# Kernel tuning notes

Measured on AMD Instinct MI355X. Metric: run time of the kernel, lower is better.

## Reference

```python
import jax, jax.numpy as jnp
import numpy as np

VOLRADIUS = 256.0
DT = 1.0 / VOLRADIUS  # self.dt = dt / volradius with dt=1.0
N_STEPS = 64
B, H, W, K, M = 1, 256, 256, 64, 16


def setup_inputs() -> dict:
    rng = np.random.default_rng(0)
    # orthographic-ish ray bundle looking down +z through the primitive cloud
    ys, xs = np.meshgrid(np.linspace(-1., 1., H, dtype=np.float32),
                         np.linspace(-1., 1., W, dtype=np.float32), indexing='ij')
    raypos = np.broadcast_to(np.stack([xs, ys, np.full_like(xs, -0.125)], -1)[None],
                             (B, H, W, 3)).astype(np.float32).copy()
    raydir = np.zeros((B, H, W, 3), np.float32); raydir[..., 2] = 1.0
    tmin = np.zeros((B, H, W), np.float32)
    tminmax = np.stack([tmin, tmin + N_STEPS * DT], -1).astype(np.float32)
    # primpos is in WORLD units (module divides by volradius)
    primpos = rng.uniform(-0.1 * VOLRADIUS, 0.1 * VOLRADIUS, (B, K, 3)).astype(np.float32)
    q, _ = np.linalg.qr(rng.normal(size=(B, K, 3, 3)))
    primrot = q.astype(np.float32)
    primscale = rng.uniform(8., 16., (B, K, 3)).astype(np.float32)  # inverse half-extent
    primrgba = rng.uniform(0., 1., (B, K, 4, M, M, M)).astype(np.float32)
    return {
        'raypos': jnp.asarray(raypos), 'raydir': jnp.asarray(raydir),
        'tminmax': jnp.asarray(tminmax), 'primpos': jnp.asarray(primpos),
        'primrot': jnp.asarray(primrot), 'primscale': jnproundtrip(primscale) if False else jnp.asarray(primscale),
        'primrgba': jnp.asarray(primrgba),
    }


def _trilinear_sum(template, pos, primpos, primrot, primscale):
    # template [K,4,M,M,M]; pos [R,3]; returns summed rgba over primitives [R,4]
    Mv = template.shape[-1]
    kidx = jnp.arange(template.shape[0])[None, :]                      # [1,K]
    rel = pos[:, None, :] - primpos[None, :, :]                        # [R,K,3]
    # local = primscale * (primrot^T @ rel), inside prim iff |local| < 1
    local = jnp.einsum('kij,rki->rkj', primrot, rel) * primscale[None]  # [R,K,3]
    inside = jnp.all(jnp.abs(local) < 1.0, axis=-1)                    # [R,K]
    g = jnp.clip((local + 1.0) * 0.5 * (Mv - 1), 0.0, Mv - 1 - 1e-5)    # voxel coords (x,y,z)
    i0 = jnp.clip(jnp.floor(g).astype(jnp.int32), 0, Mv - 2)
    f = g - i0.astype(g.dtype)
    x0, y0, z0 = i0[..., 0], i0[..., 1], i0[..., 2]
    fx, fy, fz = f[..., 0], f[..., 1], f[..., 2]
    c = jnp.zeros(local.shape[:2] + (4,), template.dtype)
    for dz, wz in ((0, 1 - fz), (1, fz)):
        for dy, wy in ((0, 1 - fy), (1, fy)):
            for dx, wx in ((0, 1 - fx), (1, fx)):
                corner = template[kidx, :, z0 + dz, y0 + dy, x0 + dx]  # [R,K,4]
                c = c + corner * (wz * wy * wx)[..., None]
    c = c * inside[..., None]
    return c.sum(axis=1)                                               # [R,4]


def _march(raypos, raydir, tminmax, primpos, primrot, primscale, template):
    Hh, Ww, _ = raypos.shape
    R = Hh * Ww
    o = raypos.reshape(R, 3)
    d = raydir.reshape(R, 3)
    tmm = tminmax.reshape(R, 2)
    tmin, tmax = tmm[:, 0], tmm[:, 1]

    def step(carry, i):
        rgb, alpha = carry
        t = tmin + (i.astype(jnp.float32) + 0.5) * DT
        valid = t < tmax
        pos = o + t[:, None] * d
        s = _trilinear_sum(template, pos, primpos, primrot, primscale)  # [R,4]
        # MVP front-to-back saturating alpha compositing (early-term equivalent)
        contrib = jnp.minimum(1.0, alpha + s[:, 3] * DT) - alpha
        contrib = jnp.where(valid, contrib, 0.0)
        rgb = rgb + s[:, :3] * contrib[:, None]
        alpha = alpha + contrib
        return (rgb, alpha), None

    init = (jnp.zeros((R, 3), jnp.float32), jnp.zeros((R,), jnp.float32))
    (rgb, alpha), _ = jax.lax.scan(jax.checkpoint(step), init, jnp.arange(N_STEPS))
    return jnp.concatenate([rgb, alpha[:, None]], -1).reshape(Hh, Ww, 4)


def reference(raypos, raydir, tminmax, primpos, primrot, primscale, primrgba):
    primpos_n = primpos / VOLRADIUS  # module normalizes primpos by volume radius
    rayrgba = jax.vmap(_march)(raypos, raydir, tminmax, primpos_n, primrot, primscale, primrgba)
    rayrgba = jnp.transpose(rayrgba, (0, 3, 1, 2))  # [B,4,H,W]
    rayrgb = rayrgba[:, :3]
    rayalpha = rayrgba[:, 3:4]
    return rayrgb, rayalpha, rayrgba
```

## Files before the change

### kernel.cpp

```cpp
#include <hip/hip_runtime.h>
#include <hip/hip_fp16.h>

#define Rtot 65536
#define Wimg 256
#define Kp 64
#define NSTEPS 64
#define DTc (1.0f/256.0f)
#define INV_VOLR (1.0f/256.0f)
#define NITEMS 16384

#define PD_OFF    0u
#define TB_OFF    4096u
#define FLAG_OFF  20480u
#define TT_OFF    65536u
#define SBUF_OFF  8388608u
#define WS_NEED   (SBUF_OFF + (size_t)NITEMS*256*8)

typedef _Float16 half2v __attribute__((ext_vector_type(2)));

__device__ __forceinline__ half2v u2h(unsigned int u) {
  union { unsigned int u; half2v h; } x; x.u = u; return x.h;
}
__device__ __forceinline__ half2v mkh2(float a, float b) {
  half2v h; h.x = (_Float16)a; h.y = (_Float16)b; return h;
}
__device__ __forceinline__ unsigned int pack2(float a, float b) {
  __half2 h = __floats2half2_rn(a, b);
  return *(unsigned int*)&h;
}

#if __has_builtin(__builtin_amdgcn_fdot2)
#define FDOT2(a, b, c) __builtin_amdgcn_fdot2((a), (b), (c), false)
#else
#define FDOT2(a, b, c) ((float)(a).x*(float)(b).x + (float)(a).y*(float)(b).y + (c))
#endif

__global__ __launch_bounds__(256) void setup_kernel(
    const float* __restrict__ raypos, const float* __restrict__ raydir,
    const float* __restrict__ tminmax, const float* __restrict__ primpos,
    const float* __restrict__ primrot, const float* __restrict__ primscale,
    const float* __restrict__ tmpl,
    float* __restrict__ tb, uint4* __restrict__ tth, float* __restrict__ pd) {
  int bid = blockIdx.x, tid = threadIdx.x;
  if (bid < 256) {
    __shared__ float smn[4][7], smx[4][7];
    int w = (bid & 15)*16 + (tid & 15);
    int h = (bid >> 4)*16 + (tid >> 4);
    int r = h*Wimg + w;
    float v[7];
    v[0] = raypos[r*3+0]; v[1] = raypos[r*3+1]; v[2] = raypos[r*3+2];
    v[3] = raydir[r*3+0]; v[4] = raydir[r*3+1]; v[5] = raydir[r*3+2];
    v[6] = tminmax[r*2+0];
    float mn[7], mx[7];
#pragma unroll
    for (int i = 0; i < 7; ++i) { mn[i] = v[i]; mx[i] = v[i]; }
#pragma unroll
    for (int m = 1; m < 64; m <<= 1) {
#pragma unroll
      for (int i = 0; i < 7; ++i) {
        mn[i] = fminf(mn[i], __shfl_xor(mn[i], m));
        mx[i] = fmaxf(mx[i], __shfl_xor(mx[i], m));
      }
    }
    int wv = tid >> 6;
    if ((tid & 63) == 0) {
#pragma unroll
      for (int i = 0; i < 7; ++i) { smn[wv][i] = mn[i]; smx[wv][i] = mx[i]; }
    }
    __syncthreads();
    if (tid == 0) {
#pragma unroll
      for (int i = 0; i < 7; ++i) {
        tb[bid*16 + i]     = fminf(fminf(smn[0][i], smn[1][i]), fminf(smn[2][i], smn[3][i]));
        tb[bid*16 + 8 + i] = fmaxf(fmaxf(smx[0][i], smx[1][i]), fmaxf(smx[2][i], smx[3][i]));
      }
    }
  } else if (bid < 320) {
    int k = bid - 256;
    const float* b0 = tmpl + (((size_t)k) << 14);
    uint4* o = tth + (k << 12);
    for (int v = tid; v < 4096; v += 256) {
      int x = v & 15;
      int xn = (x < 15) ? v + 1 : v;
      uint4 q;
      q.x = pack2(b0[v],         b0[xn]);
      q.y = pack2(b0[4096+v],    b0[4096+xn]);
      q.z = pack2(b0[8192+v],    b0[8192+xn]);
      q.w = pack2(b0[12288+v],   b0[12288+xn]);
      o[v] = q;
    }
  } else {
    int k = tid;
    if (k < Kp) {
      float sc0 = primscale[k*3+0], sc1 = primscale[k*3+1], sc2 = primscale[k*3+2];
      float* o = pd + (k << 4);
      o[0] = primpos[k*3+0] * INV_VOLR;
      o[1] = primpos[k*3+1] * INV_VOLR;
      o[2] = primpos[k*3+2] * INV_VOLR;
      o[3] = 0.0f; o[4] = 0.0f; o[5] = 0.0f;
#pragma unroll
      for (int i = 0; i < 3; ++i) {
        o[6+i*3+0] = primrot[k*9+i*3+0]*sc0;
        o[6+i*3+1] = primrot[k*9+i*3+1]*sc1;
        o[6+i*3+2] = primrot[k*9+i*3+2]*sc2;
      }
      o[15] = 0.0f;
    }
  }
}

#define PRIM_SETUP(S, kk, vm)                                                \
  { const float* p = pd + ((kk) << 4);                                       \
    float relx = px - p[0], rely = py - p[1], relz = pz - p[2];              \
    float lx = relx*p[6] + rely*p[9]  + relz*p[12];                          \
    float ly = relx*p[7] + rely*p[10] + relz*p[13];                          \
    float lz = relx*p[8] + rely*p[11] + relz*p[14];                          \
    bool inside = fabsf(lx) < 1.0f && fabsf(ly) < 1.0f && fabsf(lz) < 1.0f;  \
    float gx = fminf(fmaxf((lx + 1.0f)*7.5f, 0.0f), 14.99999f);              \
    float gy = fminf(fmaxf((ly + 1.0f)*7.5f, 0.0f), 14.99999f);              \
    float gz = fminf(fmaxf((lz + 1.0f)*7.5f, 0.0f), 14.99999f);              \
    int ix = (int)gx, iy = (int)gy, iz = (int)gz;                            \
    float fx = gx - (float)ix, fy = gy - (float)iy, fz = gz - (float)iz;     \
    float m = inside ? (vm) : 0.0f;                                          \
    float wy0 = 1.0f - fy, wz0m = (1.0f - fz)*m, fzm = fz*m;                 \
    float wx0 = 1.0f - fx;                                                   \
    float w00 = wz0m*wy0, w01 = wz0m*fy, w10 = fzm*wy0, w11 = fzm*fy;        \
    w2_0##S = mkh2(w00*wx0, w00*fx);                                         \
    w2_1##S = mkh2(w01*wx0, w01*fx);                                         \
    w2_2##S = mkh2(w10*wx0, w10*fx);                                         \
    w2_3##S = mkh2(w11*wx0, w11*fx);                                         \
    const uint4* a = tth + ((size_t)(kk) << 12) + (iz*256 + iy*16 + ix);     \
    q0##S = a[0]; q1##S = a[16]; q2##S = a[256]; q3##S = a[272]; }

#define PRIM_ACC(S)                                                          \
  { c0 = FDOT2(u2h(q0##S.x), w2_0##S, c0);                                   \
    c1 = FDOT2(u2h(q0##S.y), w2_0##S, c1);                                   \
    c2 = FDOT2(u2h(q0##S.z), w2_0##S, c2);                                   \
    c3 = FDOT2(u2h(q0##S.w), w2_0##S, c3);                                   \
    c0 = FDOT2(u2h(q1##S.x), w2_1##S, c0);                                   \
    c1 = FDOT2(u2h(q1##S.y), w2_1##S, c1);                                   \
    c2 = FDOT2(u2h(q1##S.z), w2_1##S, c2);                                   \
    c3 = FDOT2(u2h(q1##S.w), w2_1##S, c3);                                   \
    c0 = FDOT2(u2h(q2##S.x), w2_2##S, c0);                                   \
    c1 = FDOT2(u2h(q2##S.y), w2_2##S, c1);                                   \
    c2 = FDOT2(u2h(q2##S.z), w2_2##S, c2);                                   \
    c3 = FDOT2(u2h(q2##S.w), w2_2##S, c3);                                   \
    c0 = FDOT2(u2h(q3##S.x), w2_3##S, c0);                                   \
    c1 = FDOT2(u2h(q3##S.y), w2_3##S, c1);                                   \
    c2 = FDOT2(u2h(q3##S.z), w2_3##S, c2);                                   \
    c3 = FDOT2(u2h(q3##S.w), w2_3##S, c3); }

__global__ __launch_bounds__(256) void shade_kernel(
    const float* __restrict__ raypos, const float* __restrict__ raydir,
    const float* __restrict__ tminmax, const float* __restrict__ pd,
    const float* __restrict__ tb, const uint4* __restrict__ tth,
    unsigned long long* __restrict__ sbuf, unsigned char* __restrict__ flags) {
  __shared__ int s_any;
  __shared__ int s_list[4][66];
  int item = blockIdx.x;
  int tile = item >> 6, step = item & 63;
  int tid = threadIdx.x;
  int lane = tid & 63, wv = tid >> 6;

  if (tid < 64) {
    const float* t0 = tb + tile*16;
    float cst = ((float)step + 0.5f)*DTc;
    float tl = t0[6] + cst, th = t0[14] + cst;
    const float* p = pd + (tid << 4);
    float rlo[3], rhi[3];
#pragma unroll
    for (int a = 0; a < 3; ++a) {
      float ol = t0[a], oh = t0[8+a], dl = t0[3+a], dh = t0[11+a];
      float p1 = tl*dl, p2 = tl*dh, p3 = th*dl, p4 = th*dh;
      rlo[a] = ol + fminf(fminf(p1, p2), fminf(p3, p4)) - p[a];
      rhi[a] = oh + fmaxf(fmaxf(p1, p2), fmaxf(p3, p4)) - p[a];
    }
    bool pass = true;
#pragma unroll
    for (int j = 0; j < 3; ++j) {
      float llo = 0.f, lhi = 0.f;
#pragma unroll
      for (int a = 0; a < 3; ++a) {
        float rsc = p[6+a*3+j];
        float q1 = rlo[a]*rsc, q2 = rhi[a]*rsc;
        llo += fminf(q1, q2);
        lhi += fmaxf(q1, q2);
      }
      pass = pass && (llo < 1.0f) && (lhi > -1.0f);
    }
    unsigned long long mask = __ballot(pass);
    if (tid == 0) s_any = (mask != 0ull);
  }
  __syncthreads();
  if (!s_any) {
    if (tid == 0) flags[item] = 0;
    return;
  }
  if (tid == 0) flags[item] = 1;

  int w = (tile & 15)*16 + (tid & 15);
  int h = (tile >> 4)*16 + (tid >> 4);
  int r = h*Wimg + w;
  float t = tminmax[r*2] + ((float)step + 0.5f)*DTc;
  float px = fmaf(t, raydir[r*3+0], raypos[r*3+0]);
  float py = fmaf(t, raydir[r*3+1], raypos[r*3+1]);
  float pz = fmaf(t, raydir[r*3+2], raypos[r*3+2]);

  float bmnx = px, bmny = py, bmnz = pz, bmxx = px, bmxy = py, bmxz = pz;
#pragma unroll
  for (int m = 1; m < 64; m <<= 1) {
    bmnx = fminf(bmnx, __shfl_xor(bmnx, m));
    bmny = fminf(bmny, __shfl_xor(bmny, m));
    bmnz = fminf(bmnz, __shfl_xor(bmnz, m));
    bmxx = fmaxf(bmxx, __shfl_xor(bmxx, m));
    bmxy = fmaxf(bmxy, __shfl_xor(bmxy, m));
    bmxz = fmaxf(bmxz, __shfl_xor(bmxz, m));
  }
  {
    const float* p = pd + (lane << 4);
    float rlo0 = bmnx - p[0], rhi0 = bmxx - p[0];
    float rlo1 = bmny - p[1], rhi1 = bmxy - p[1];
    float rlo2 = bmnz - p[2], rhi2 = bmxz - p[2];
    bool pass = true;
#pragma unroll
    for (int j = 0; j < 3; ++j) {
      float a0 = p[6+j], a1 = p[9+j], a2 = p[12+j];
      float q1 = rlo0*a0, q2 = rhi0*a0;
      float llo = fminf(q1, q2), lhi = fmaxf(q1, q2);
      q1 = rlo1*a1; q2 = rhi1*a1;
      llo += fminf(q1, q2); lhi += fmaxf(q1, q2);
      q1 = rlo2*a2; q2 = rhi2*a2;
      llo += fminf(q1, q2); lhi += fmaxf(q1, q2);
      pass = pass && (llo < 1.0f) && (lhi > -1.0f);
    }
    unsigned long long mask = __ballot(pass);
    int cnt = (int)__popcll(mask);
    if (pass) {
      int pos = (int)__popcll(mask & ((1ull << lane) - 1ull));
      s_list[wv][pos] = lane;
    }
    int cntp = ((cnt + 2) / 3) * 3;
    if (lane < cntp - cnt) s_list[wv][cnt + lane] = 0;

    float c0 = 0.f, c1 = 0.f, c2 = 0.f, c3 = 0.f;
    if (cnt > 0) {
      bool anyA, anyB, anyC; (void)anyA; (void)anyB; (void)anyC;
      uint4 q0A, q1A, q2A, q3A, q0B, q1B, q2B, q3B, q0C, q1C, q2C, q3C;
      half2v w2_0A, w2_1A, w2_2A, w2_3A;
      half2v w2_0B, w2_1B, w2_2B, w2_3B;
      half2v w2_0C, w2_1C, w2_2C, w2_3C;
      int kk = __builtin_amdgcn_readfirstlane(s_list[wv][0]);
      PRIM_SETUP(A, kk, 1.0f)
      kk = __builtin_amdgcn_readfirstlane(s_list[wv][1]);
      PRIM_SETUP(B, kk, (1 < cnt) ? 1.0f : 0.0f)
      kk = __builtin_amdgcn_readfirstlane(s_list[wv][2]);
      PRIM_SETUP(C, kk, (2 < cnt) ? 1.0f : 0.0f)
      for (int i = 3; i + 2 < cntp; i += 3) {
        PRIM_ACC(A)
        kk = __builtin_amdgcn_readfirstlane(s_list[wv][i]);
        PRIM_SETUP(A, kk, (i < cnt) ? 1.0f : 0.0f)
        PRIM_ACC(B)
        kk = __builtin_amdgcn_readfirstlane(s_list[wv][i+1]);
        PRIM_SETUP(B, kk, (i+1 < cnt) ? 1.0f : 0.0f)
        PRIM_ACC(C)
        kk = __builtin_amdgcn_readfirstlane(s_list[wv][i+2]);
        PRIM_SETUP(C, kk, (i+2 < cnt) ? 1.0f : 0.0f)
      }
      PRIM_ACC(A)
      PRIM_ACC(B)
      PRIM_ACC(C)
    }
    unsigned long long pk = ((unsigned long long)pack2(c2, c3) << 32)
                          | (unsigned long long)pack2(c0, c1);
    sbuf[item*256 + tid] = pk;
  }
}

__global__ __launch_bounds__(256) void composite_kernel(
    const float* __restrict__ tminmax, const unsigned long long* __restrict__ sbuf,
    const unsigned char* __restrict__ flags, float* __restrict__ out) {
  __shared__ unsigned char s_flags[NSTEPS];
  int tid = threadIdx.x;
  int b = blockIdx.x;
  if (tid < NSTEPS) s_flags[tid] = flags[b*NSTEPS + tid];
  __syncthreads();
  int w = (b & 15)*16 + (tid & 15);
  int h = (b >> 4)*16 + (tid >> 4);
  int r = h*Wimg + w;
  float tmin = tminmax[r*2+0], tmax = tminmax[r*2+1];
  float rgb0 = 0.f, rgb1 = 0.f, rgb2 = 0.f, alpha = 0.f;
  for (int i = 0; i < NSTEPS; ++i) {
    float s0 = 0.f, s1 = 0.f, s2 = 0.f, s3 = 0.f;
    if (s_flags[i]) {
      unsigned long long pk = sbuf[(b*NSTEPS + i)*256 + tid];
      unsigned int lo = (unsigned int)pk, hi = (unsigned int)(pk >> 32);
      float2 lf = __half22float2(*(__half2*)&lo);
      float2 hf = __half22float2(*(__half2*)&hi);
      s0 = lf.x; s1 = lf.y; s2 = hf.x; s3 = hf.y;
    }
    float t = tmin + ((float)i + 0.5f)*DTc;
    float contrib = fminf(1.0f, fmaf(s3, DTc, alpha)) - alpha;
    contrib = (t < tmax) ? contrib : 0.0f;
    rgb0 = fmaf(s0, contrib, rgb0);
    rgb1 = fmaf(s1, contrib, rgb1);
    rgb2 = fmaf(s2, contrib, rgb2);
    alpha += contrib;
  }
  out[0*Rtot + r] = rgb0;
  out[1*Rtot + r] = rgb1;
  out[2*Rtot + r] = rgb2;
  out[3*Rtot + r] = alpha;
  out[4*Rtot + r] = rgb0;
  out[5*Rtot + r] = rgb1;
  out[6*Rtot + r] = rgb2;
  out[7*Rtot + r] = alpha;
}

__global__ __launch_bounds__(256) void fallback_kernel(
    const float* __restrict__ raypos, const float* __restrict__ raydir,
    const float* __restrict__ tminmax,
    const float* __restrict__ primpos, const float* __restrict__ primrot,
    const float* __restrict__ primscale, const float* __restrict__ tmpl,
    float* __restrict__ out) {
  __shared__ float s_pd[Kp][16];
  int tx = threadIdx.x, ty = threadIdx.y;
  int tid = ty*16 + tx;
  if (tid < Kp) {
    int k = tid;
    float sc0 = primscale[k*3+0], sc1 = primscale[k*3+1], sc2 = primscale[k*3+2];
    s_pd[k][0] = primpos[k*3+0]*INV_VOLR;
    s_pd[k][1] = primpos[k*3+1]*INV_VOLR;
    s_pd[k][2] = primpos[k*3+2]*INV_VOLR;
#pragma unroll
    for (int i = 0; i < 3; ++i) {
      s_pd[k][6+i*3+0] = primrot[k*9+i*3+0]*sc0;
      s_pd[k][6+i*3+1] = primrot[k*9+i*3+1]*sc1;
      s_pd[k][6+i*3+2] = primrot[k*9+i*3+2]*sc2;
    }
  }
  __syncthreads();
  int w = blockIdx.x*16 + tx, h = blockIdx.y*16 + ty;
  int r = h*Wimg + w;
  float ox = raypos[r*3+0], oy = raypos[r*3+1], oz = raypos[r*3+2];
  float dx = raydir[r*3+0], dy = raydir[r*3+1], dz = raydir[r*3+2];
  float tmin = tminmax[r*2+0], tmax = tminmax[r*2+1];
  float rgb0=0.f, rgb1=0.f, rgb2=0.f, alpha=0.f;
  for (int i = 0; i < NSTEPS; ++i) {
    float t = tmin + ((float)i + 0.5f)*DTc;
    float px = fmaf(t, dx, ox), py = fmaf(t, dy, oy), pz = fmaf(t, dz, oz);
    float c[4] = {0.f, 0.f, 0.f, 0.f};
    for (int k = 0; k < Kp; ++k) {
      const float* p = &s_pd[k][0];
      float relx = px - p[0], rely = py - p[1], relz = pz - p[2];
      float lx = relx*p[6] + rely*p[9]  + relz*p[12];
      float ly = relx*p[7] + rely*p[10] + relz*p[13];
      float lz = relx*p[8] + rely*p[11] + relz*p[14];
      if (!(fabsf(lx) < 1.0f && fabsf(ly) < 1.0f && fabsf(lz) < 1.0f)) continue;
      float gx = fminf(fmaxf((lx + 1.0f)*7.5f, 0.0f), 14.99999f);
      float gy = fminf(fmaxf((ly + 1.0f)*7.5f, 0.0f), 14.99999f);
      float gz = fminf(fmaxf((lz + 1.0f)*7.5f, 0.0f), 14.99999f);
      int ix = (int)gx, iy = (int)gy, iz = (int)gz;
      ix = ix > 14 ? 14 : ix; iy = iy > 14 ? 14 : iy; iz = iz > 14 ? 14 : iz;
      float fx = gx - (float)ix, fy = gy - (float)iy, fz = gz - (float)iz;
      float wx0 = 1.0f - fx, wy0 = 1.0f - fy, wz0 = 1.0f - fz;
      float w00 = wz0*wy0, w01 = wz0*fy, w10 = fz*wy0, w11 = fz*fy;
      const float* base = tmpl + (((size_t)k) << 14) + iz*256 + iy*16 + ix;
#pragma unroll
      for (int ch = 0; ch < 4; ++ch) {
        const float* bb = base + ch*4096;
        c[ch] += (bb[0]  *wx0 + bb[1]  *fx) * w00
               + (bb[16] *wx0 + bb[17] *fx) * w01
               + (bb[256]*wx0 + bb[257]*fx) * w10
               + (bb[272]*wx0 + bb[273]*fx) * w11;
      }
    }
    float contrib = fminf(1.0f, fmaf(c[3], DTc, alpha)) - alpha;
    contrib = (t < tmax) ? contrib : 0.0f;
    rgb0 = fmaf(c[0], contrib, rgb0);
    rgb1 = fmaf(c[1], contrib, rgb1);
    rgb2 = fmaf(c[2], contrib, rgb2);
    alpha += contrib;
  }
  out[0*Rtot + r] = rgb0;
  out[1*Rtot + r] = rgb1;
  out[2*Rtot + r] = rgb2;
  out[3*Rtot + r] = alpha;
  out[4*Rtot + r] = rgb0;
  out[5*Rtot + r] = rgb1;
  out[6*Rtot + r] = rgb2;
  out[7*Rtot + r] = alpha;
}

extern "C" void kernel_launch(void* const* d_in, const int* in_sizes, int n_in,
                              void* d_out, int out_size, void* d_ws, size_t ws_size,
                              hipStream_t stream) {
  const float* raypos    = (const float*)d_in[0];
  const float* raydir    = (const float*)d_in[1];
  const float* tminmax   = (const float*)d_in[2];
  const float* primpos   = (const float*)d_in[3];
  const float* primrot   = (const float*)d_in[4];
  const float* primscale = (const float*)d_in[5];
  const float* primrgba  = (const float*)d_in[6];
  float* out = (float*)d_out;

  if (ws_size >= WS_NEED) {
    char* ws = (char*)d_ws;
    float* pd            = (float*)(ws + PD_OFF);
    float* tb            = (float*)(ws + TB_OFF);
    unsigned char* flags = (unsigned char*)(ws + FLAG_OFF);
    uint4* tth           = (uint4*)(ws + TT_OFF);
    unsigned long long* sbuf = (unsigned long long*)(ws + SBUF_OFF);

    setup_kernel<<<321, 256, 0, stream>>>(raypos, raydir, tminmax, primpos,
                                          primrot, primscale, primrgba,
                                          tb, tth, pd);
    shade_kernel<<<NITEMS, 256, 0, stream>>>(raypos, raydir, tminmax, pd, tb,
                                             tth, sbuf, flags);
    composite_kernel<<<256, 256, 0, stream>>>(tminmax, sbuf, flags, out);
  } else {
    fallback_kernel<<<dim3(16,16), dim3(16,16), 0, stream>>>(
        raypos, raydir, tminmax, primpos, primrot, primscale, primrgba, out);
  }
}
```

Before: 73.43 us.

## Split tile culling into separate kernel and shade compacted work queue persistently

```diff
diff --git a/kernel.cpp b/kernel.cpp
--- a/kernel.cpp
+++ b/kernel.cpp
@@ -8,11 +8,15 @@
 #define DTc (1.0f/256.0f)
 #define INV_VOLR (1.0f/256.0f)
 #define NITEMS 16384
+#define HOTGRID 2048
 
 #define PD_OFF    0u
 #define TB_OFF    4096u
 #define FLAG_OFF  20480u
-#define TT_OFF    65536u
+#define QC_OFF    36864u
+#define QUEUE_OFF 40960u
+#define LIST_OFF  131072u
+#define TT_OFF    2097152u
 #define SBUF_OFF  8388608u
 #define WS_NEED   (SBUF_OFF + (size_t)NITEMS*256*8)
 
@@ -40,7 +44,8 @@
     const float* __restrict__ tminmax, const float* __restrict__ primpos,
     const float* __restrict__ primrot, const float* __restrict__ primscale,
     const float* __restrict__ tmpl,
-    float* __restrict__ tb, uint4* __restrict__ tth, float* __restrict__ pd) {
+    float* __restrict__ tb, uint4* __restrict__ tth, float* __restrict__ pd,
+    int* __restrict__ qc) {
   int bid = blockIdx.x, tid = threadIdx.x;
   if (bid < 256) {
     __shared__ float smn[4][7], smx[4][7];
@@ -75,22 +80,26 @@
         tb[bid*16 + 8 + i] = fmaxf(fmaxf(smx[0][i], smx[1][i]), fmaxf(smx[2][i], smx[3][i]));
       }
     }
-  } else if (bid < 320) {
-    int k = bid - 256;
+  } else if (bid < 512) {
+    int k = (bid - 256) >> 2;
+    int q = (bid - 256) & 3;
     const float* b0 = tmpl + (((size_t)k) << 14);
     uint4* o = tth + (k << 12);
-    for (int v = tid; v < 4096; v += 256) {
+#pragma unroll
+    for (int s = 0; s < 4; ++s) {
+      int v = q*1024 + s*256 + tid;
       int x = v & 15;
       int xn = (x < 15) ? v + 1 : v;
-      uint4 q;
-      q.x = pack2(b0[v],         b0[xn]);
-      q.y = pack2(b0[4096+v],    b0[4096+xn]);
-      q.z = pack2(b0[8192+v],    b0[8192+xn]);
-      q.w = pack2(b0[12288+v],   b0[12288+xn]);
-      o[v] = q;
+      uint4 qq;
+      qq.x = pack2(b0[v],       b0[xn]);
+      qq.y = pack2(b0[4096+v],  b0[4096+xn]);
+      qq.z = pack2(b0[8192+v],  b0[8192+xn]);
+      qq.w = pack2(b0[12288+v], b0[12288+xn]);
+      o[v] = qq;
     }
   } else {
     int k = tid;
+    if (k == Kp) qc[0] = 0;
     if (k < Kp) {
       float sc0 = primscale[k*3+0], sc1 = primscale[k*3+1], sc2 = primscale[k*3+2];
       float* o = pd + (k << 4);
@@ -106,6 +115,51 @@
       }
       o[15] = 0.0f;
     }
+  }
+}
+
+__global__ __launch_bounds__(256) void cull_kernel(
+    const float* __restrict__ pd, const float* __restrict__ tb,
+    unsigned char* __restrict__ flags, unsigned char* __restrict__ lists,
+    int* __restrict__ queue, int* __restrict__ qc) {
+  int wv = threadIdx.x >> 6, lane = threadIdx.x & 63;
+  int item = blockIdx.x*4 + wv;
+  int tile = item >> 6, step = item & 63;
+  const float* t0 = tb + tile*16;
+  float cst = ((float)step + 0.5f)*DTc;
+  float tl = t0[6] + cst, th = t0[14] + cst;
+  const float* p = pd + (lane << 4);
+  float rlo[3], rhi[3];
+#pragma unroll
+  for (int a = 0; a < 3; ++a) {
+    float ol = t0[a], oh = t0[8+a], dl = t0[3+a], dh = t0[11+a];
+    float p1 = tl*dl, p2 = tl*dh, p3 = th*dl, p4 = th*dh;
+    rlo[a] = ol + fminf(fminf(p1, p2), fminf(p3, p4)) - p[a];
+    rhi[a] = oh + fmaxf(fmaxf(p1, p2), fmaxf(p3, p4)) - p[a];
+  }
+  bool pass = true;
+#pragma unroll
+  for (int j = 0; j < 3; ++j) {
+    float llo = 0.f, lhi = 0.f;
+#pragma unroll
+    for (int a = 0; a < 3; ++a) {
+      float rsc = p[6+a*3+j];
+      float q1 = rlo[a]*rsc, q2 = rhi[a]*rsc;
+      llo += fminf(q1, q2);
+      lhi += fmaxf(q1, q2);
+    }
+    pass = pass && (llo < 1.0f) && (lhi > -1.0f);
+  }
+  unsigned long long mask = __ballot(pass);
+  int cnt = (int)__popcll(mask);
+  if (lane == 0) flags[item] = (unsigned char)(cnt > 0 ? 1 : 0);
+  if (pass) {
+    int pos = (int)__popcll(mask & ((1ull << lane) - 1ull));
+    lists[item*64 + pos] = (unsigned char)lane;
+  }
+  if (cnt > 0 && lane == 0) {
+    int qpos = atomicAdd(qc, 1);
+    queue[qpos] = item | (cnt << 16);
   }
 }
 
@@ -153,98 +207,67 @@
 __global__ __launch_bounds__(256) void shade_kernel(
     const float* __restrict__ raypos, const float* __restrict__ raydir,
     const float* __restrict__ tminmax, const float* __restrict__ pd,
-    const float* __restrict__ tb, const uint4* __restrict__ tth,
-    unsigned long long* __restrict__ sbuf, unsigned char* __restrict__ flags) {
-  __shared__ int s_any;
+    const uint4* __restrict__ tth, const unsigned char* __restrict__ lists,
+    const int* __restrict__ queue, const int* __restrict__ qc,
+    unsigned long long* __restrict__ sbuf) {
   __shared__ int s_list[4][66];
-  int item = blockIdx.x;
-  int tile = item >> 6, step = item & 63;
+  int qn = qc[0];
   int tid = threadIdx.x;
   int lane = tid & 63, wv = tid >> 6;
-
-  if (tid < 64) {
-    const float* t0 = tb + tile*16;
-    float cst = ((float)step + 0.5f)*DTc;
-    float tl = t0[6] + cst, th = t0[14] + cst;
-    const float* p = pd + (tid << 4);
-    float rlo[3], rhi[3];
-#pragma unroll
-    for (int a = 0; a < 3; ++a) {
-      float ol = t0[a], oh = t0[8+a], dl = t0[3+a], dh = t0[11+a];
-      float p1 = tl*dl, p2 = tl*dh, p3 = th*dl, p4 = th*dh;
-      rlo[a] = ol + fminf(fminf(p1, p2), fminf(p3, p4)) - p[a];
-      rhi[a] = oh + fmaxf(fmaxf(p1, p2), fmaxf(p3, p4)) - p[a];
-    }
-    bool pass = true;
-#pragma unroll
-    for (int j = 0; j < 3; ++j) {
-      float llo = 0.f, lhi = 0.f;
-#pragma unroll
-      for (int a = 0; a < 3; ++a) {
-        float rsc = p[6+a*3+j];
-        float q1 = rlo[a]*rsc, q2 = rhi[a]*rsc;
-        llo += fminf(q1, q2);
-        lhi += fmaxf(q1, q2);
-      }
-      pass = pass && (llo < 1.0f) && (lhi > -1.0f);
-    }
-    unsigned long long mask = __ballot(pass);
-    if (tid == 0) s_any = (mask != 0ull);
-  }
-  __syncthreads();
-  if (!s_any) {
-    if (tid == 0) flags[item] = 0;
-    return;
-  }
-  if (tid == 0) flags[item] = 1;
-
-  int w = (tile & 15)*16 + (tid & 15);
-  int h = (tile >> 4)*16 + (tid >> 4);
-  int r = h*Wimg + w;
-  float t = tminmax[r*2] + ((float)step + 0.5f)*DTc;
-  float px = fmaf(t, raydir[r*3+0], raypos[r*3+0]);
-  float py = fmaf(t, raydir[r*3+1], raypos[r*3+1]);
-  float pz = fmaf(t, raydir[r*3+2], raypos[r*3+2]);
-
-  float bmnx = px, bmny = py, bmnz = pz, bmxx = px, bmxy = py, bmxz = pz;
-#pragma unroll
-  for (int m = 1; m < 64; m <<= 1) {
-    bmnx = fminf(bmnx, __shfl_xor(bmnx, m));
-    bmny = fminf(bmny, __shfl_xor(bmny, m));
-    bmnz = fminf(bmnz, __shfl_xor(bmnz, m));
-    bmxx = fmaxf(bmxx, __shfl_xor(bmxx, m));
-    bmxy = fmaxf(bmxy, __shfl_xor(bmxy, m));
-    bmxz = fmaxf(bmxz, __shfl_xor(bmxz, m));
-  }
-  {
-    const float* p = pd + (lane << 4);
-    float rlo0 = bmnx - p[0], rhi0 = bmxx - p[0];
-    float rlo1 = bmny - p[1], rhi1 = bmxy - p[1];
-    float rlo2 = bmnz - p[2], rhi2 = bmxz - p[2];
-    bool pass = true;
-#pragma unroll
-    for (int j = 0; j < 3; ++j) {
-      float a0 = p[6+j], a1 = p[9+j], a2 = p[12+j];
-      float q1 = rlo0*a0, q2 = rhi0*a0;
-      float llo = fminf(q1, q2), lhi = fmaxf(q1, q2);
-      q1 = rlo1*a1; q2 = rhi1*a1;
-      llo += fminf(q1, q2); lhi += fmaxf(q1, q2);
-      q1 = rlo2*a2; q2 = rhi2*a2;
-      llo += fminf(q1, q2); lhi += fmaxf(q1, q2);
-      pass = pass && (llo < 1.0f) && (lhi > -1.0f);
+  for (int it = blockIdx.x; it < qn; it += HOTGRID) {
+    int entry = queue[it];
+    int item = entry & 0xFFFF;
+    int cnt0 = entry >> 16;
+    int tile = item >> 6, step = item & 63;
+    int w = (tile & 15)*16 + (tid & 15);
+    int h = (tile >> 4)*16 + (tid >> 4);
+    int r = h*Wimg + w;
+    float t = tminmax[r*2] + ((float)step + 0.5f)*DTc;
+    float px = fmaf(t, raydir[r*3+0], raypos[r*3+0]);
+    float py = fmaf(t, raydir[r*3+1], raypos[r*3+1]);
+    float pz = fmaf(t, raydir[r*3+2], raypos[r*3+2]);
+
+    float bmnx = px, bmny = py, bmnz = pz, bmxx = px, bmxy = py, bmxz = pz;
+#pragma unroll
+    for (int m = 1; m < 64; m <<= 1) {
+      bmnx = fminf(bmnx, __shfl_xor(bmnx, m));
+      bmny = fminf(bmny, __shfl_xor(bmny, m));
+      bmnz = fminf(bmnz, __shfl_xor(bmnz, m));
+      bmxx = fmaxf(bmxx, __shfl_xor(bmxx, m));
+      bmxy = fmaxf(bmxy, __shfl_xor(bmxy, m));
+      bmxz = fmaxf(bmxz, __shfl_xor(bmxz, m));
+    }
+    int kk0 = (lane < cnt0) ? (int)lists[item*64 + lane] : 0;
+    bool pass = false;
+    if (lane < cnt0) {
+      const float* p = pd + (kk0 << 4);
+      float rlo0 = bmnx - p[0], rhi0 = bmxx - p[0];
+      float rlo1 = bmny - p[1], rhi1 = bmxy - p[1];
+      float rlo2 = bmnz - p[2], rhi2 = bmxz - p[2];
+      pass = true;
+#pragma unroll
+      for (int j = 0; j < 3; ++j) {
+        float a0 = p[6+j], a1 = p[9+j], a2 = p[12+j];
+        float q1 = rlo0*a0, q2 = rhi0*a0;
+        float llo = fminf(q1, q2), lhi = fmaxf(q1, q2);
+        q1 = rlo1*a1; q2 = rhi1*a1;
+        llo += fminf(q1, q2); lhi += fmaxf(q1, q2);
+        q1 = rlo2*a2; q2 = rhi2*a2;
+        llo += fminf(q1, q2); lhi += fmaxf(q1, q2);
+        pass = pass && (llo < 1.0f) && (lhi > -1.0f);
+      }
     }
     unsigned long long mask = __ballot(pass);
     int cnt = (int)__popcll(mask);
     if (pass) {
       int pos = (int)__popcll(mask & ((1ull << lane) - 1ull));
-      s_list[wv][pos] = lane;
+      s_list[wv][pos] = kk0;
     }
     int cntp = ((cnt + 2) / 3) * 3;
     if (lane < cntp - cnt) s_list[wv][cnt + lane] = 0;
 
     float c0 = 0.f, c1 = 0.f, c2 = 0.f, c3 = 0.f;
     if (cnt > 0) {
-      bool anyA, anyB, anyC; (void)anyA; (void)anyB; (void)anyC;
       uint4 q0A, q1A, q2A, q3A, q0B, q1B, q2B, q3B, q0C, q1C, q2C, q3C;
       half2v w2_0A, w2_1A, w2_2A, w2_3A;
       half2v w2_0B, w2_1B, w2_2B, w2_3B;
@@ -408,14 +431,18 @@
     float* pd            = (float*)(ws + PD_OFF);
     float* tb            = (float*)(ws + TB_OFF);
     unsigned char* flags = (unsigned char*)(ws + FLAG_OFF);
+    int* qc              = (int*)(ws + QC_OFF);
+    int* queue           = (int*)(ws + QUEUE_OFF);
+    unsigned char* lists = (unsigned char*)(ws + LIST_OFF);
     uint4* tth           = (uint4*)(ws + TT_OFF);
     unsigned long long* sbuf = (unsigned long long*)(ws + SBUF_OFF);
 
-    setup_kernel<<<321, 256, 0, stream>>>(raypos, raydir, tminmax, primpos,
+    setup_kernel<<<513, 256, 0, stream>>>(raypos, raydir, tminmax, primpos,
                                           primrot, primscale, primrgba,
-                                          tb, tth, pd);
-    shade_kernel<<<NITEMS, 256, 0, stream>>>(raypos, raydir, tminmax, pd, tb,
-                                             tth, sbuf, flags);
+                                          tb, tth, pd, qc);
+    cull_kernel<<<NITEMS/4, 256, 0, stream>>>(pd, tb, flags, lists, queue, qc);
+    shade_kernel<<<HOTGRID, 256, 0, stream>>>(raypos, raydir, tminmax, pd,
+                                              tth, lists, queue, qc, sbuf);
     composite_kernel<<<256, 256, 0, stream>>>(tminmax, sbuf, flags, out);
   } else {
     fallback_kernel<<<dim3(16,16), dim3(16,16), 0, stream>>>(
```

New measurement: 86.47 us. 1.18x slower.
